# Kernel tuning notes

Measured on AMD Instinct MI355X. Metric: run time of the kernel, lower is better.

## Reference

```python
import jax, jax.numpy as jnp
import numpy as np

N, E, DIN, DOUT = 50000, 800000, 64, 64


def setup_inputs() -> dict:
    key = jax.random.key(0)
    k1, k2, k3, k4, k5 = jax.random.split(key, 5)
    x = jax.random.normal(k1, (N, DIN), dtype=jnp.float32)
    edge_index = jax.random.randint(k2, (2, E), 0, N, dtype=jnp.int64)
    edge_attr = jax.random.uniform(k3, (E,), dtype=jnp.float32)
    # PyG GCNConv params: linear weight (no bias in lin) + conv bias
    W = jax.random.normal(k4, (DIN, DOUT), dtype=jnp.float32) / np.sqrt(DIN)
    b = jax.random.normal(k5, (DOUT,), dtype=jnp.float32) * 0.01
    return {
        "x": x,
        "edge_index": edge_index,
        "edge_attr": edge_attr,
        "return_attention_weights": 0,
        "W": W,
        "b": b,
    }


def reference(x, edge_index, edge_attr, return_attention_weights, W, b):
    # GCNConv(add_self_loops=False, normalize=True), edge_weight = ones.
    # edge_attr / return_attention_weights are unused by the original module.
    n = x.shape[0]
    src, dst = edge_index[0], edge_index[1]
    # in-degree on destination nodes (gcn_norm with ones edge weights)
    deg = jax.ops.segment_sum(jnp.ones_like(src, dtype=x.dtype), dst, num_segments=n)
    dis = jnp.where(deg > 0, jax.lax.rsqrt(jnp.maximum(deg, 1)), jnp.zeros_like(deg))
    norm = dis[src] * dis[dst]  # [E]
    h = x @ W  # [N, DOUT] -- transform before aggregation (in < out would flip, equal here)
    msg = h[src] * norm[:, None]  # [E, DOUT]
    out = jax.ops.segment_sum(msg, dst, num_segments=n) + b  # [N, DOUT]
    return out
```

## Files before the change

### kernel.cpp

```cpp
#include <hip/hip_runtime.h>
#include <stdint.h>


#define CAP   64
#define BSH   7
#define NBMAX 512
#define EPB   4096
#define BCAP  2816

typedef float vf4 __attribute__((ext_vector_type(4)));

__device__ __forceinline__ int probe_is64(const void* eidx, int n_edges, int n_nodes) {
    int lane = threadIdx.x & 63;
    const long long* p = (const long long*)eidx;
    int cnt = n_edges < 64 ? n_edges : 64;
    long long v = p[lane % cnt];
    bool ok = (v >= 0) && (v < (long long)n_nodes);
    return (__ballot(ok) == ~0ull) ? 1 : 0;
}

__device__ __forceinline__ int load_idx(const void* eidx, long long i, int is64) {
    if (is64) return (int)((const long long*)eidx)[i];
    return ((const int*)eidx)[i];
}

__device__ __forceinline__ unsigned short f2bf(float v) {
    unsigned u = __float_as_uint(v);
    unsigned r = (u + 0x7fffu + ((u >> 16) & 1u)) >> 16;
    return (unsigned short)r;
}

__device__ __forceinline__ float bflo(unsigned u) { return __uint_as_float(u << 16); }
__device__ __forceinline__ float bfhi(unsigned u) { return __uint_as_float(u & 0xffff0000u); }

__global__ __launch_bounds__(256) void k_bin(
    const void* eidx, unsigned* __restrict__ tails,
    unsigned* __restrict__ buckets, int n, int ne, int nb)
{
    __shared__ unsigned histo[NBMAX];
    __shared__ unsigned base[NBMAX];
    const int tid = (int)threadIdx.x;
    for (int i = tid; i < NBMAX; i += 256) histo[i] = 0;
    int is64 = probe_is64(eidx, ne, n);
    __syncthreads();

    unsigned pk[16], rk[16];
    long long e0 = (long long)blockIdx.x * EPB + tid;
    #pragma unroll
    for (int j = 0; j < 16; ++j) {
        long long e = e0 + 256 * j;
        if (e < (long long)ne) {
            int s = load_idx(eidx, e, is64);
            int t = load_idx(eidx, (long long)ne + e, is64);
            pk[j] = ((unsigned)t << 16) | (unsigned)s;
            rk[j] = atomicAdd(&histo[(unsigned)t >> BSH], 1u);
        } else {
            pk[j] = 0u; rk[j] = 0xFFFFFFFFu;
        }
    }
    __syncthreads();
    unsigned U = tails[NBMAX];
    for (int b = tid; b < nb; b += 256) {
        unsigned c = histo[b];
        base[b] = c ? (atomicAdd(&tails[b], c) - U) : 0u;
    }
    __syncthreads();
    #pragma unroll
    for (int j = 0; j < 16; ++j) {
        if (rk[j] != 0xFFFFFFFFu) {
            unsigned bk = pk[j] >> (16 + BSH);
            unsigned slot = base[bk] + rk[j];
            if (slot < (unsigned)BCAP)
                buckets[(size_t)bk * BCAP + slot] = pk[j];
        }
    }
}

__global__ __launch_bounds__(256) void k_place2(
    const unsigned* __restrict__ tails,
    const unsigned* __restrict__ buckets,
    unsigned short* __restrict__ csr16,
    float* __restrict__ dis, unsigned char* __restrict__ endc, int n)
{
    __shared__ unsigned degL[1 << BSH];
    const int tid = (int)threadIdx.x;
    const int b = (int)blockIdx.x;
    const int t0 = b << BSH;
    if (tid < (1 << BSH)) degL[tid] = 0;
    __syncthreads();
    unsigned U = tails[NBMAX];
    unsigned cnt = tails[b] - U;
    if (cnt > (unsigned)BCAP) cnt = (unsigned)BCAP;
    for (unsigned i = (unsigned)tid; i < cnt; i += 256) {
        unsigned p = buckets[(size_t)b * BCAP + i];
        unsigned dl = (p >> 16) & ((1u << BSH) - 1);
        unsigned r = atomicAdd(&degL[dl], 1u);
        if (r < (unsigned)CAP)
            csr16[((size_t)(t0 + (int)dl)) * CAP + r] = (unsigned short)(p & 0xFFFFu);
    }
    __syncthreads();
    if (tid < (1 << BSH)) {
        int node = t0 + tid;
        if (node < n) {
            unsigned d = degL[tid];
            dis[node] = d ? rsqrtf((float)d) : 0.f;
            endc[node] = (unsigned char)(d < (unsigned)CAP ? d : (unsigned)CAP);
        }
    }
}

__global__ __launch_bounds__(256) void k_place_direct(
    const void* eidx, unsigned* __restrict__ deg,
    unsigned short* __restrict__ csr16, int n, int ne)
{
    int is64 = probe_is64(eidx, ne, n);
    unsigned base = deg[n];
    int e = (int)blockIdx.x * 256 + (int)threadIdx.x;
    if (e >= ne) return;
    int s = load_idx(eidx, e, is64);
    int t = load_idx(eidx, (long long)ne + e, is64);
    unsigned r = atomicAdd(&deg[t], 1u) - base;
    if (r < (unsigned)CAP)
        csr16[(size_t)t * CAP + r] = (unsigned short)s;
}

__global__ __launch_bounds__(256) void k_finalize_direct(
    const unsigned* __restrict__ deg,
    float* __restrict__ dis, unsigned char* __restrict__ endc, int n)
{
    int i = (int)blockIdx.x * 256 + (int)threadIdx.x;
    if (i >= n) return;
    unsigned base = deg[n];
    unsigned cnt = deg[i] - base;
    dis[i] = cnt ? rsqrtf((float)cnt) : 0.f;
    endc[i] = (unsigned char)(cnt < (unsigned)CAP ? cnt : (unsigned)CAP);
}

__global__ __launch_bounds__(256) void k_gemm(
    const float* __restrict__ x, const float* __restrict__ W,
    uint2* __restrict__ hlo, uint2* __restrict__ hhi, int n)
{
    __shared__ float Ws[64 * 64];
    __shared__ float xsT[64 * 68];
    const int t = (int)threadIdx.x;
    const int row0 = (int)blockIdx.x * 64;

    for (int j = 0; j < 4; ++j) {
        int q = t + 256 * j;
        float4 w4 = ((const float4*)W)[q];
        float* d = &Ws[q * 4];
        d[0] = w4.x; d[1] = w4.y; d[2] = w4.z; d[3] = w4.w;
    }
    for (int j = 0; j < 4; ++j) {
        int q = t + 256 * j;
        int r = q >> 4, c4 = (q & 15) * 4;
        int row = row0 + r;
        float4 v4 = (row < n) ? ((const float4*)x)[(size_t)row * 16 + (q & 15)]
                              : make_float4(0.f, 0.f, 0.f, 0.f);
        xsT[(c4 + 0) * 68 + r] = v4.x;
        xsT[(c4 + 1) * 68 + r] = v4.y;
        xsT[(c4 + 2) * 68 + r] = v4.z;
        xsT[(c4 + 3) * 68 + r] = v4.w;
    }
    __syncthreads();

    const int fg = t & 15, rg = t >> 4;
    float acc[4][4];
    #pragma unroll
    for (int i = 0; i < 4; ++i)
        for (int j = 0; j < 4; ++j) acc[i][j] = 0.f;

    #pragma unroll 4
    for (int k = 0; k < 64; ++k) {
        vf4 w4 = *(const vf4*)&Ws[k * 64 + fg * 4];
        vf4 x4 = *(const vf4*)&xsT[k * 68 + rg * 4];
        #pragma unroll
        for (int i = 0; i < 4; ++i) {
            acc[i][0] += x4[i] * w4.x;
            acc[i][1] += x4[i] * w4.y;
            acc[i][2] += x4[i] * w4.z;
            acc[i][3] += x4[i] * w4.w;
        }
    }
    const int rbase = row0 + rg * 4;
    #pragma unroll
    for (int i = 0; i < 4; ++i) {
        int row = rbase + i;
        if (row < n) {
            uint2 u;
            u.x = (unsigned)f2bf(acc[i][0]) | ((unsigned)f2bf(acc[i][1]) << 16);
            u.y = (unsigned)f2bf(acc[i][2]) | ((unsigned)f2bf(acc[i][3]) << 16);
            if (fg < 8) hlo[(size_t)row * 8 + fg]       = u;
            else        hhi[(size_t)row * 8 + (fg - 8)] = u;
        }
    }
}

__global__ __launch_bounds__(256) void k_aggregate(
    const float* __restrict__ dis,
    const unsigned char* __restrict__ endc,
    const unsigned short* __restrict__ csr16,
    const uint2* __restrict__ hlo, const uint2* __restrict__ hhi,
    const float* __restrict__ bias,
    float* __restrict__ out, int n)
{
    int wid  = (int)threadIdx.x >> 6;
    int lane = (int)threadIdx.x & 63;
    int t = ((int)blockIdx.x >> 1) * 4 + wid;
    int half = (int)blockIdx.x & 1;
    if (t >= n) return;
    const uint2* __restrict__ h = half ? hhi : hlo;

    int allsrc = (int)csr16[(size_t)t * CAP + lane];
    unsigned end = endc[t];
    float dis_t = dis[t];
    int f = lane & 7, oct = lane >> 3;
    float a0 = 0.f, a1 = 0.f, a2 = 0.f, a3 = 0.f;

    unsigned K16 = end >> 4;
    for (unsigned k = 0; k < K16; ++k) {
        int j = (int)(k << 4) + oct;
        int sa = __shfl(allsrc, j, 64);
        int sb = __shfl(allsrc, j + 8, 64);
        float wa = dis[sa], wb = dis[sb];
        uint2 ua = h[(size_t)sa * 8 + f];
        uint2 ub = h[(size_t)sb * 8 + f];
        a0 += wa * bflo(ua.x) + wb * bflo(ub.x);
        a1 += wa * bfhi(ua.x) + wb * bfhi(ub.x);
        a2 += wa * bflo(ua.y) + wb * bflo(ub.y);
        a3 += wa * bfhi(ua.y) + wb * bfhi(ub.y);
    }
    unsigned done = K16 << 4;
    if (end & 8u) {
        int j = (int)done + oct;
        int s = __shfl(allsrc, j, 64);
        float w = dis[s];
        uint2 u = h[(size_t)s * 8 + f];
        a0 += w * bflo(u.x); a1 += w * bfhi(u.x);
        a2 += w * bflo(u.y); a3 += w * bfhi(u.y);
        done += 8;
    }
    unsigned rem = end & 7u;
    if (rem) {
        unsigned jj = done + (unsigned)oct;
        bool valid = jj < end;
        int s = __shfl(allsrc, (int)(jj & 63u), 64);
        s = valid ? s : 0;
        float w = valid ? dis[s] : 0.f;
        uint2 u = h[(size_t)s * 8 + f];
        a0 += w * bflo(u.x); a1 += w * bfhi(u.x);
        a2 += w * bflo(u.y); a3 += w * bfhi(u.y);
    }
    a0 += __shfl_xor(a0, 8, 64); a0 += __shfl_xor(a0, 16, 64); a0 += __shfl_xor(a0, 32, 64);
    a1 += __shfl_xor(a1, 8, 64); a1 += __shfl_xor(a1, 16, 64); a1 += __shfl_xor(a1, 32, 64);
    a2 += __shfl_xor(a2, 8, 64); a2 += __shfl_xor(a2, 16, 64); a2 += __shfl_xor(a2, 32, 64);
    a3 += __shfl_xor(a3, 8, 64); a3 += __shfl_xor(a3, 16, 64); a3 += __shfl_xor(a3, 32, 64);
    if (oct == 0) {
        float4 bb = ((const float4*)bias)[half * 8 + f];
        vf4 o;
        o.x = a0 * dis_t + bb.x;
        o.y = a1 * dis_t + bb.y;
        o.z = a2 * dis_t + bb.z;
        o.w = a3 * dis_t + bb.w;
        ((vf4*)out)[(size_t)t * 16 + half * 8 + f] = o;
    }
}

extern "C" void kernel_launch(void* const* d_in, const int* in_sizes, int n_in,
                              void* d_out, int out_size, void* d_ws, size_t ws_size,
                              hipStream_t stream) {
    const float* x   = (const float*)d_in[0];
    const void* eidx = d_in[1];
    const float* W   = (const float*)d_in[4];
    const float* b   = (const float*)d_in[5];
    float* out       = (float*)d_out;

    const int n  = in_sizes[0] / 64;
    const int ne = in_sizes[2];
    const int nb = (n + (1 << BSH) - 1) >> BSH;

    auto al = [](size_t v) { return (v + 255) & ~(size_t)255; };

    size_t need = al((size_t)(NBMAX + 1) * 4) + al((size_t)nb * BCAP * 4)
                + al((size_t)n * CAP * 2) + 2 * al((size_t)n * 16 * 4)
                + al((size_t)n * 4) + al((size_t)n);
    bool binned = (ws_size >= need) && (nb <= NBMAX);

    char* base = (char*)d_ws;
    size_t off = 0;
    unsigned*       tails   = (unsigned*)(base + off);     off = al(off + (size_t)(NBMAX + 1) * 4);
    unsigned*       buckets = (unsigned*)(base + off);     off = al(off + (size_t)nb * BCAP * 4);
    unsigned short* csr16   = (unsigned short*)(base + off); off = al(off + (size_t)n * CAP * 2);
    uint2*          hlo     = (uint2*)(base + off);        off = al(off + (size_t)n * 16 * 4);
    uint2*          hhi     = (uint2*)(base + off);        off = al(off + (size_t)n * 16 * 4);
    float*          dis     = (float*)(base + off);        off = al(off + (size_t)n * 4);
    unsigned char*  endc    = (unsigned char*)(base + off); off = al(off + (size_t)n);

    if (binned) {
        k_bin<<<(ne + EPB - 1) / EPB, 256, 0, stream>>>(eidx, tails, buckets, n, ne, nb);
        k_place2<<<nb, 256, 0, stream>>>(tails, buckets, csr16, dis, endc, n);
    } else {
        unsigned* deg = buckets;
        k_place_direct<<<(ne + 255) / 256, 256, 0, stream>>>(eidx, deg, csr16, n, ne);
        k_finalize_direct<<<(n + 255) / 256, 256, 0, stream>>>(deg, dis, endc, n);
    }
    k_gemm<<<(n + 63) / 64, 256, 0, stream>>>(x, W, hlo, hhi, n);
    k_aggregate<<<2 * ((n + 3) / 4), 256, 0, stream>>>(dis, endc, csr16, hlo, hhi, b, out, n);
}
```

Measured before the change: 137.1 us.

## Fuse binning, GEMM, CSR placement and aggregation into one cooperative persistent kernel

Replaces the four separate launches with a single persistent cooperative kernel of fixed grid size. Its phases are separated by grid-wide syncs, with edge binning and the x@W GEMM running concurrently on disjoint block subsets. Bucket granularity is halved (64 nodes per bucket, more buckets) so placement has more parallel blocks. The intent is to remove launch gaps and overlap the GEMM with binning, at the cost of grid.sync overhead, limited occupancy in the aggregation phase, and a fallback path with three launches. The direct non-binned fallback is also removed.

```diff
diff --git a/kernel.cpp b/kernel.cpp
--- a/kernel.cpp
+++ b/kernel.cpp
@@ -1,12 +1,16 @@
 #include <hip/hip_runtime.h>
+#include <hip/hip_cooperative_groups.h>
 #include <stdint.h>
 
+namespace cg = cooperative_groups;
+
 
 #define CAP   64
-#define BSH   7
-#define NBMAX 512
+#define BSH   6
+#define NBMAX 1024
 #define EPB   4096
-#define BCAP  2816
+#define BCAP  1408
+#define GRID  1024
 
 typedef float vf4 __attribute__((ext_vector_type(4)));
 
@@ -33,236 +37,211 @@
 __device__ __forceinline__ float bflo(unsigned u) { return __uint_as_float(u << 16); }
 __device__ __forceinline__ float bfhi(unsigned u) { return __uint_as_float(u & 0xffff0000u); }
 
-__global__ __launch_bounds__(256) void k_bin(
-    const void* eidx, unsigned* __restrict__ tails,
-    unsigned* __restrict__ buckets, int n, int ne, int nb)
+__global__ __launch_bounds__(256, 4) void k_mega(
+    const float* __restrict__ x, const void* eidx,
+    const float* __restrict__ W, const float* __restrict__ bias,
+    float* __restrict__ out,
+    unsigned* __restrict__ tails, unsigned* __restrict__ buckets,
+    unsigned short* __restrict__ csr16,
+    uint2* __restrict__ hlo, uint2* __restrict__ hhi,
+    float* __restrict__ dis, unsigned char* __restrict__ endc,
+    int n, int ne, int nb, int nchunks, int binb, int phases)
 {
-    __shared__ unsigned histo[NBMAX];
-    __shared__ unsigned base[NBMAX];
+    union SM {
+        struct { unsigned histo[NBMAX]; unsigned base[NBMAX]; } bin;
+        struct { float Ws[64 * 64]; float xsT[64 * 68]; } gm;
+        unsigned degL[1 << BSH];
+    };
+    __shared__ SM sm;
     const int tid = (int)threadIdx.x;
-    for (int i = tid; i < NBMAX; i += 256) histo[i] = 0;
-    int is64 = probe_is64(eidx, ne, n);
-    __syncthreads();
-
-    unsigned pk[16], rk[16];
-    long long e0 = (long long)blockIdx.x * EPB + tid;
-    #pragma unroll
-    for (int j = 0; j < 16; ++j) {
-        long long e = e0 + 256 * j;
-        if (e < (long long)ne) {
-            int s = load_idx(eidx, e, is64);
-            int t = load_idx(eidx, (long long)ne + e, is64);
-            pk[j] = ((unsigned)t << 16) | (unsigned)s;
-            rk[j] = atomicAdd(&histo[(unsigned)t >> BSH], 1u);
+    const int bid = (int)blockIdx.x;
+
+    if (phases & 1) {
+        if (bid < binb) {
+            int is64 = probe_is64(eidx, ne, n);
+            for (int c = bid; c < nchunks; c += binb) {
+                __syncthreads();
+                for (int i = tid; i < NBMAX; i += 256) sm.bin.histo[i] = 0u;
+                __syncthreads();
+                unsigned pk[16], rk[16];
+                long long e0 = (long long)c * EPB + tid;
+                #pragma unroll
+                for (int j = 0; j < 16; ++j) {
+                    long long e = e0 + 256 * j;
+                    if (e < (long long)ne) {
+                        int s = load_idx(eidx, e, is64);
+                        int t = load_idx(eidx, (long long)ne + e, is64);
+                        pk[j] = ((unsigned)t << 16) | (unsigned)s;
+                        rk[j] = atomicAdd(&sm.bin.histo[(unsigned)t >> BSH], 1u);
+                    } else { pk[j] = 0u; rk[j] = 0xFFFFFFFFu; }
+                }
+                __syncthreads();
+                unsigned U = tails[NBMAX];
+                for (int b2 = tid; b2 < nb; b2 += 256) {
+                    unsigned cc = sm.bin.histo[b2];
+                    sm.bin.base[b2] = cc ? (atomicAdd(&tails[b2], cc) - U) : 0u;
+                }
+                __syncthreads();
+                #pragma unroll
+                for (int j = 0; j < 16; ++j) {
+                    if (rk[j] != 0xFFFFFFFFu) {
+                        unsigned bk = pk[j] >> (16 + BSH);
+                        unsigned slot = sm.bin.base[bk] + rk[j];
+                        if (slot < (unsigned)BCAP)
+                            buckets[(size_t)bk * BCAP + slot] = pk[j];
+                    }
+                }
+            }
         } else {
-            pk[j] = 0u; rk[j] = 0xFFFFFFFFu;
+            const int gb = (int)gridDim.x - binb;
+            const int ntiles = (n + 63) >> 6;
+            for (int j = 0; j < 4; ++j) {
+                int q = tid + 256 * j;
+                float4 w4 = ((const float4*)W)[q];
+                float* d = &sm.gm.Ws[q * 4];
+                d[0] = w4.x; d[1] = w4.y; d[2] = w4.z; d[3] = w4.w;
+            }
+            const int fg = tid & 15, rg = tid >> 4;
+            for (int tile = bid - binb; tile < ntiles; tile += gb) {
+                __syncthreads();
+                int row0 = tile << 6;
+                for (int j = 0; j < 4; ++j) {
+                    int q = tid + 256 * j;
+                    int r = q >> 4, c4 = (q & 15) * 4;
+                    int row = row0 + r;
+                    float4 v4 = (row < n) ? ((const float4*)x)[(size_t)row * 16 + (q & 15)]
+                                          : make_float4(0.f, 0.f, 0.f, 0.f);
+                    sm.gm.xsT[(c4 + 0) * 68 + r] = v4.x;
+                    sm.gm.xsT[(c4 + 1) * 68 + r] = v4.y;
+                    sm.gm.xsT[(c4 + 2) * 68 + r] = v4.z;
+                    sm.gm.xsT[(c4 + 3) * 68 + r] = v4.w;
+                }
+                __syncthreads();
+                float acc[4][4];
+                #pragma unroll
+                for (int i = 0; i < 4; ++i)
+                    #pragma unroll
+                    for (int j2 = 0; j2 < 4; ++j2) acc[i][j2] = 0.f;
+                #pragma unroll 4
+                for (int k = 0; k < 64; ++k) {
+                    vf4 w4 = *(const vf4*)&sm.gm.Ws[k * 64 + fg * 4];
+                    vf4 x4 = *(const vf4*)&sm.gm.xsT[k * 68 + rg * 4];
+                    #pragma unroll
+                    for (int i = 0; i < 4; ++i) {
+                        acc[i][0] += x4[i] * w4.x;
+                        acc[i][1] += x4[i] * w4.y;
+                        acc[i][2] += x4[i] * w4.z;
+                        acc[i][3] += x4[i] * w4.w;
+                    }
+                }
+                int rbase = row0 + rg * 4;
+                #pragma unroll
+                for (int i = 0; i < 4; ++i) {
+                    int row = rbase + i;
+                    if (row < n) {
+                        uint2 u;
+                        u.x = (unsigned)f2bf(acc[i][0]) | ((unsigned)f2bf(acc[i][1]) << 16);
+                        u.y = (unsigned)f2bf(acc[i][2]) | ((unsigned)f2bf(acc[i][3]) << 16);
+                        if (fg < 8) hlo[(size_t)row * 8 + fg]       = u;
+                        else        hhi[(size_t)row * 8 + (fg - 8)] = u;
+                    }
+                }
+            }
         }
     }
-    __syncthreads();
-    unsigned U = tails[NBMAX];
-    for (int b = tid; b < nb; b += 256) {
-        unsigned c = histo[b];
-        base[b] = c ? (atomicAdd(&tails[b], c) - U) : 0u;
-    }
-    __syncthreads();
-    #pragma unroll
-    for (int j = 0; j < 16; ++j) {
-        if (rk[j] != 0xFFFFFFFFu) {
-            unsigned bk = pk[j] >> (16 + BSH);
-            unsigned slot = base[bk] + rk[j];
-            if (slot < (unsigned)BCAP)
-                buckets[(size_t)bk * BCAP + slot] = pk[j];
+    cg::grid_group grid = cg::this_grid();
+    if ((phases & 3) == 3) grid.sync();
+
+    if (phases & 2) {
+        for (int b2 = bid; b2 < nb; b2 += (int)gridDim.x) {
+            __syncthreads();
+            if (tid < (1 << BSH)) sm.degL[tid] = 0u;
+            __syncthreads();
+            unsigned U = tails[NBMAX];
+            unsigned cnt = tails[b2] - U;
+            if (cnt > (unsigned)BCAP) cnt = (unsigned)BCAP;
+            int t0 = b2 << BSH;
+            for (unsigned i = (unsigned)tid; i < cnt; i += 256) {
+                unsigned p = buckets[(size_t)b2 * BCAP + i];
+                unsigned dl = (p >> 16) & ((1u << BSH) - 1);
+                unsigned r = atomicAdd(&sm.degL[dl], 1u);
+                if (r < (unsigned)CAP)
+                    csr16[((size_t)(t0 + (int)dl)) * CAP + r] = (unsigned short)(p & 0xFFFFu);
+            }
+            __syncthreads();
+            if (tid < (1 << BSH)) {
+                int node = t0 + tid;
+                if (node < n) {
+                    unsigned d = sm.degL[tid];
+                    dis[node] = d ? rsqrtf((float)d) : 0.f;
+                    endc[node] = (unsigned char)(d < (unsigned)CAP ? d : (unsigned)CAP);
+                }
+            }
         }
     }
-}
-
-__global__ __launch_bounds__(256) void k_place2(
-    const unsigned* __restrict__ tails,
-    const unsigned* __restrict__ buckets,
-    unsigned short* __restrict__ csr16,
-    float* __restrict__ dis, unsigned char* __restrict__ endc, int n)
-{
-    __shared__ unsigned degL[1 << BSH];
-    const int tid = (int)threadIdx.x;
-    const int b = (int)blockIdx.x;
-    const int t0 = b << BSH;
-    if (tid < (1 << BSH)) degL[tid] = 0;
-    __syncthreads();
-    unsigned U = tails[NBMAX];
-    unsigned cnt = tails[b] - U;
-    if (cnt > (unsigned)BCAP) cnt = (unsigned)BCAP;
-    for (unsigned i = (unsigned)tid; i < cnt; i += 256) {
-        unsigned p = buckets[(size_t)b * BCAP + i];
-        unsigned dl = (p >> 16) & ((1u << BSH) - 1);
-        unsigned r = atomicAdd(&degL[dl], 1u);
-        if (r < (unsigned)CAP)
-            csr16[((size_t)(t0 + (int)dl)) * CAP + r] = (unsigned short)(p & 0xFFFFu);
-    }
-    __syncthreads();
-    if (tid < (1 << BSH)) {
-        int node = t0 + tid;
-        if (node < n) {
-            unsigned d = degL[tid];
-            dis[node] = d ? rsqrtf((float)d) : 0.f;
-            endc[node] = (unsigned char)(d < (unsigned)CAP ? d : (unsigned)CAP);
+    if ((phases & 6) == 6) grid.sync();
+
+    if (phases & 4) {
+        const int wid = tid >> 6, lane = tid & 63;
+        const int f = lane & 7, oct = lane >> 3;
+        const int nvirt = 2 * ((n + 3) / 4);
+        for (int v = bid; v < nvirt; v += (int)gridDim.x) {
+            int t = (v >> 1) * 4 + wid;
+            int half = v & 1;
+            if (t < n) {
+                const uint2* __restrict__ h = half ? hhi : hlo;
+                int allsrc = (int)csr16[(size_t)t * CAP + lane];
+                unsigned end = endc[t];
+                float dis_t = dis[t];
+                float a0 = 0.f, a1 = 0.f, a2 = 0.f, a3 = 0.f;
+                unsigned K16 = end >> 4;
+                for (unsigned k = 0; k < K16; ++k) {
+                    int j = (int)(k << 4) + oct;
+                    int sa = __shfl(allsrc, j, 64);
+                    int sb = __shfl(allsrc, j + 8, 64);
+                    float wa = dis[sa], wb = dis[sb];
+                    uint2 ua = h[(size_t)sa * 8 + f];
+                    uint2 ub = h[(size_t)sb * 8 + f];
+                    a0 += wa * bflo(ua.x) + wb * bflo(ub.x);
+                    a1 += wa * bfhi(ua.x) + wb * bfhi(ub.x);
+                    a2 += wa * bflo(ua.y) + wb * bflo(ub.y);
+                    a3 += wa * bfhi(ua.y) + wb * bfhi(ub.y);
+                }
+                unsigned done = K16 << 4;
+                if (end & 8u) {
+                    int j = (int)done + oct;
+                    int s = __shfl(allsrc, j, 64);
+                    float w = dis[s];
+                    uint2 u = h[(size_t)s * 8 + f];
+                    a0 += w * bflo(u.x); a1 += w * bfhi(u.x);
+                    a2 += w * bflo(u.y); a3 += w * bfhi(u.y);
+                    done += 8;
+                }
+                if (end & 7u) {
+                    unsigned jj = done + (unsigned)oct;
+                    bool valid = jj < end;
+                    int s = __shfl(allsrc, (int)(jj & 63u), 64);
+                    s = valid ? s : 0;
+                    float w = valid ? dis[s] : 0.f;
+                    uint2 u = h[(size_t)s * 8 + f];
+                    a0 += w * bflo(u.x); a1 += w * bfhi(u.x);
+                    a2 += w * bflo(u.y); a3 += w * bfhi(u.y);
+                }
+                a0 += __shfl_xor(a0, 8, 64); a0 += __shfl_xor(a0, 16, 64); a0 += __shfl_xor(a0, 32, 64);
+                a1 += __shfl_xor(a1, 8, 64); a1 += __shfl_xor(a1, 16, 64); a1 += __shfl_xor(a1, 32, 64);
+                a2 += __shfl_xor(a2, 8, 64); a2 += __shfl_xor(a2, 16, 64); a2 += __shfl_xor(a2, 32, 64);
+                a3 += __shfl_xor(a3, 8, 64); a3 += __shfl_xor(a3, 16, 64); a3 += __shfl_xor(a3, 32, 64);
+                if (oct == 0) {
+                    float4 bb = ((const float4*)bias)[half * 8 + f];
+                    vf4 o;
+                    o.x = a0 * dis_t + bb.x;
+                    o.y = a1 * dis_t + bb.y;
+                    o.z = a2 * dis_t + bb.z;
+                    o.w = a3 * dis_t + bb.w;
+                    ((vf4*)out)[(size_t)t * 16 + half * 8 + f] = o;
+                }
+            }
         }
-    }
-}
-
-__global__ __launch_bounds__(256) void k_place_direct(
-    const void* eidx, unsigned* __restrict__ deg,
-    unsigned short* __restrict__ csr16, int n, int ne)
-{
-    int is64 = probe_is64(eidx, ne, n);
-    unsigned base = deg[n];
-    int e = (int)blockIdx.x * 256 + (int)threadIdx.x;
-    if (e >= ne) return;
-    int s = load_idx(eidx, e, is64);
-    int t = load_idx(eidx, (long long)ne + e, is64);
-    unsigned r = atomicAdd(&deg[t], 1u) - base;
-    if (r < (unsigned)CAP)
-        csr16[(size_t)t * CAP + r] = (unsigned short)s;
-}
-
-__global__ __launch_bounds__(256) void k_finalize_direct(
-    const unsigned* __restrict__ deg,
-    float* __restrict__ dis, unsigned char* __restrict__ endc, int n)
-{
-    int i = (int)blockIdx.x * 256 + (int)threadIdx.x;
-    if (i >= n) return;
-    unsigned base = deg[n];
-    unsigned cnt = deg[i] - base;
-    dis[i] = cnt ? rsqrtf((float)cnt) : 0.f;
-    endc[i] = (unsigned char)(cnt < (unsigned)CAP ? cnt : (unsigned)CAP);
-}
-
-__global__ __launch_bounds__(256) void k_gemm(
-    const float* __restrict__ x, const float* __restrict__ W,
-    uint2* __restrict__ hlo, uint2* __restrict__ hhi, int n)
-{
-    __shared__ float Ws[64 * 64];
-    __shared__ float xsT[64 * 68];
-    const int t = (int)threadIdx.x;
-    const int row0 = (int)blockIdx.x * 64;
-
-    for (int j = 0; j < 4; ++j) {
-        int q = t + 256 * j;
-        float4 w4 = ((const float4*)W)[q];
-        float* d = &Ws[q * 4];
-        d[0] = w4.x; d[1] = w4.y; d[2] = w4.z; d[3] = w4.w;
-    }
-    for (int j = 0; j < 4; ++j) {
-        int q = t + 256 * j;
-        int r = q >> 4, c4 = (q & 15) * 4;
-        int row = row0 + r;
-        float4 v4 = (row < n) ? ((const float4*)x)[(size_t)row * 16 + (q & 15)]
-                              : make_float4(0.f, 0.f, 0.f, 0.f);
-        xsT[(c4 + 0) * 68 + r] = v4.x;
-        xsT[(c4 + 1) * 68 + r] = v4.y;
-        xsT[(c4 + 2) * 68 + r] = v4.z;
-        xsT[(c4 + 3) * 68 + r] = v4.w;
-    }
-    __syncthreads();
-
-    const int fg = t & 15, rg = t >> 4;
-    float acc[4][4];
-    #pragma unroll
-    for (int i = 0; i < 4; ++i)
-        for (int j = 0; j < 4; ++j) acc[i][j] = 0.f;
-
-    #pragma unroll 4
-    for (int k = 0; k < 64; ++k) {
-        vf4 w4 = *(const vf4*)&Ws[k * 64 + fg * 4];
-        vf4 x4 = *(const vf4*)&xsT[k * 68 + rg * 4];
-        #pragma unroll
-        for (int i = 0; i < 4; ++i) {
-            acc[i][0] += x4[i] * w4.x;
-            acc[i][1] += x4[i] * w4.y;
-            acc[i][2] += x4[i] * w4.z;
-            acc[i][3] += x4[i] * w4.w;
-        }
-    }
-    const int rbase = row0 + rg * 4;
-    #pragma unroll
-    for (int i = 0; i < 4; ++i) {
-        int row = rbase + i;
-        if (row < n) {
-            uint2 u;
-            u.x = (unsigned)f2bf(acc[i][0]) | ((unsigned)f2bf(acc[i][1]) << 16);
-            u.y = (unsigned)f2bf(acc[i][2]) | ((unsigned)f2bf(acc[i][3]) << 16);
-            if (fg < 8) hlo[(size_t)row * 8 + fg]       = u;
-            else        hhi[(size_t)row * 8 + (fg - 8)] = u;
-        }
-    }
-}
-
-__global__ __launch_bounds__(256) void k_aggregate(
-    const float* __restrict__ dis,
-    const unsigned char* __restrict__ endc,
-    const unsigned short* __restrict__ csr16,
-    const uint2* __restrict__ hlo, const uint2* __restrict__ hhi,
-    const float* __restrict__ bias,
-    float* __restrict__ out, int n)
-{
-    int wid  = (int)threadIdx.x >> 6;
-    int lane = (int)threadIdx.x & 63;
-    int t = ((int)blockIdx.x >> 1) * 4 + wid;
-    int half = (int)blockIdx.x & 1;
-    if (t >= n) return;
-    const uint2* __restrict__ h = half ? hhi : hlo;
-
-    int allsrc = (int)csr16[(size_t)t * CAP + lane];
-    unsigned end = endc[t];
-    float dis_t = dis[t];
-    int f = lane & 7, oct = lane >> 3;
-    float a0 = 0.f, a1 = 0.f, a2 = 0.f, a3 = 0.f;
-
-    unsigned K16 = end >> 4;
-    for (unsigned k = 0; k < K16; ++k) {
-        int j = (int)(k << 4) + oct;
-        int sa = __shfl(allsrc, j, 64);
-        int sb = __shfl(allsrc, j + 8, 64);
-        float wa = dis[sa], wb = dis[sb];
-        uint2 ua = h[(size_t)sa * 8 + f];
-        uint2 ub = h[(size_t)sb * 8 + f];
-        a0 += wa * bflo(ua.x) + wb * bflo(ub.x);
-        a1 += wa * bfhi(ua.x) + wb * bfhi(ub.x);
-        a2 += wa * bflo(ua.y) + wb * bflo(ub.y);
-        a3 += wa * bfhi(ua.y) + wb * bfhi(ub.y);
-    }
-    unsigned done = K16 << 4;
-    if (end & 8u) {
-        int j = (int)done + oct;
-        int s = __shfl(allsrc, j, 64);
-        float w = dis[s];
-        uint2 u = h[(size_t)s * 8 + f];
-        a0 += w * bflo(u.x); a1 += w * bfhi(u.x);
-        a2 += w * bflo(u.y); a3 += w * bfhi(u.y);
-        done += 8;
-    }
-    unsigned rem = end & 7u;
-    if (rem) {
-        unsigned jj = done + (unsigned)oct;
-        bool valid = jj < end;
-        int s = __shfl(allsrc, (int)(jj & 63u), 64);
-        s = valid ? s : 0;
-        float w = valid ? dis[s] : 0.f;
-        uint2 u = h[(size_t)s * 8 + f];
-        a0 += w * bflo(u.x); a1 += w * bfhi(u.x);
-        a2 += w * bflo(u.y); a3 += w * bfhi(u.y);
-    }
-    a0 += __shfl_xor(a0, 8, 64); a0 += __shfl_xor(a0, 16, 64); a0 += __shfl_xor(a0, 32, 64);
-    a1 += __shfl_xor(a1, 8, 64); a1 += __shfl_xor(a1, 16, 64); a1 += __shfl_xor(a1, 32, 64);
-    a2 += __shfl_xor(a2, 8, 64); a2 += __shfl_xor(a2, 16, 64); a2 += __shfl_xor(a2, 32, 64);
-    a3 += __shfl_xor(a3, 8, 64); a3 += __shfl_xor(a3, 16, 64); a3 += __shfl_xor(a3, 32, 64);
-    if (oct == 0) {
-        float4 bb = ((const float4*)bias)[half * 8 + f];
-        vf4 o;
-        o.x = a0 * dis_t + bb.x;
-        o.y = a1 * dis_t + bb.y;
-        o.z = a2 * dis_t + bb.z;
-        o.w = a3 * dis_t + bb.w;
-        ((vf4*)out)[(size_t)t * 16 + half * 8 + f] = o;
     }
 }
 
@@ -278,32 +257,48 @@
     const int n  = in_sizes[0] / 64;
     const int ne = in_sizes[2];
     const int nb = (n + (1 << BSH) - 1) >> BSH;
+    const int nchunks = (ne + EPB - 1) / EPB;
+    const int binb = nchunks < (GRID * 2 / 5) ? nchunks : (GRID * 2 / 5);
 
     auto al = [](size_t v) { return (v + 255) & ~(size_t)255; };
-
-    size_t need = al((size_t)(NBMAX + 1) * 4) + al((size_t)nb * BCAP * 4)
-                + al((size_t)n * CAP * 2) + 2 * al((size_t)n * 16 * 4)
-                + al((size_t)n * 4) + al((size_t)n);
-    bool binned = (ws_size >= need) && (nb <= NBMAX);
-
     char* base = (char*)d_ws;
     size_t off = 0;
-    unsigned*       tails   = (unsigned*)(base + off);     off = al(off + (size_t)(NBMAX + 1) * 4);
-    unsigned*       buckets = (unsigned*)(base + off);     off = al(off + (size_t)nb * BCAP * 4);
+    unsigned*       tails   = (unsigned*)(base + off);       off = al(off + (size_t)(NBMAX + 1) * 4);
+    unsigned*       buckets = (unsigned*)(base + off);       off = al(off + (size_t)nb * BCAP * 4);
     unsigned short* csr16   = (unsigned short*)(base + off); off = al(off + (size_t)n * CAP * 2);
-    uint2*          hlo     = (uint2*)(base + off);        off = al(off + (size_t)n * 16 * 4);
-    uint2*          hhi     = (uint2*)(base + off);        off = al(off + (size_t)n * 16 * 4);
-    float*          dis     = (float*)(base + off);        off = al(off + (size_t)n * 4);
-    unsigned char*  endc    = (unsigned char*)(base + off); off = al(off + (size_t)n);
-
-    if (binned) {
-        k_bin<<<(ne + EPB - 1) / EPB, 256, 0, stream>>>(eidx, tails, buckets, n, ne, nb);
-        k_place2<<<nb, 256, 0, stream>>>(tails, buckets, csr16, dis, endc, n);
-    } else {
-        unsigned* deg = buckets;
-        k_place_direct<<<(ne + 255) / 256, 256, 0, stream>>>(eidx, deg, csr16, n, ne);
-        k_finalize_direct<<<(n + 255) / 256, 256, 0, stream>>>(deg, dis, endc, n);
-    }
-    k_gemm<<<(n + 63) / 64, 256, 0, stream>>>(x, W, hlo, hhi, n);
-    k_aggregate<<<2 * ((n + 3) / 4), 256, 0, stream>>>(dis, endc, csr16, hlo, hhi, b, out, n);
-}
+    uint2*          hlo     = (uint2*)(base + off);          off = al(off + (size_t)n * 16 * 4);
+    uint2*          hhi     = (uint2*)(base + off);          off = al(off + (size_t)n * 16 * 4);
+    float*          dis     = (float*)(base + off);          off = al(off + (size_t)n * 4);
+    unsigned char*  endc    = (unsigned char*)(base + off);  off = al(off + (size_t)n);
+    (void)ws_size;
+
+    static int coop_ok = -1;
+    if (coop_ok < 0) {
+        int dev = 0; hipGetDevice(&dev);
+        int sup = 0; hipDeviceGetAttribute(&sup, hipDeviceAttributeCooperativeLaunch, dev);
+        int ncu = 0; hipDeviceGetAttribute(&ncu, hipDeviceAttributeMultiprocessorCount, dev);
+        int mb  = 0;
+        hipOccupancyMaxActiveBlocksPerMultiprocessor(&mb, k_mega, 256, 0);
+        coop_ok = (sup && (long long)mb * ncu >= GRID) ? 1 : 0;
+    }
+
+    int n_ = n, ne_ = ne, nb_ = nb, nc_ = nchunks, bb_ = binb;
+    if (coop_ok) {
+        int ph = 7;
+        void* kargs[] = {
+            (void*)&x, (void*)&eidx, (void*)&W, (void*)&b, (void*)&out,
+            (void*)&tails, (void*)&buckets, (void*)&csr16, (void*)&hlo, (void*)&hhi,
+            (void*)&dis, (void*)&endc, (void*)&n_, (void*)&ne_, (void*)&nb_,
+            (void*)&nc_, (void*)&bb_, (void*)&ph };
+        hipError_t err = hipLaunchCooperativeKernel((const void*)k_mega,
+                              dim3(GRID), dim3(256), kargs, 0, stream);
+        if (err == hipSuccess) return;
+        coop_ok = 0;
+    }
+    k_mega<<<GRID, 256, 0, stream>>>(x, eidx, W, b, out, tails, buckets, csr16,
+                                     hlo, hhi, dis, endc, n, ne, nb, nchunks, binb, 1);
+    k_mega<<<GRID, 256, 0, stream>>>(x, eidx, W, b, out, tails, buckets, csr16,
+                                     hlo, hhi, dis, endc, n, ne, nb, nchunks, binb, 2);
+    k_mega<<<GRID, 256, 0, stream>>>(x, eidx, W, b, out, tails, buckets, csr16,
+                                     hlo, hhi, dis, endc, n, ne, nb, nchunks, binb, 4);
+}
```

Result: no change. 139.4 us (+1.7%).
